# Kernel optimization log

Hardware: AMD Instinct MI355X
Metric: run time of the kernel (lower is better)

The kernel has to match this reference:

```python
import jax, jax.numpy as jnp
import numpy as np

B, S, D = 16, 512, 1024
H, HD = 16, 64          # head, head_dim; attn_dim = H*HD = D
FF = 4096               # linear_dim
EPS = 1e-6              # flax LayerNorm default epsilon


def _layernorm(x, scale):
    # flax LayerNorm(use_bias=False, use_scale=True)
    m = jnp.mean(x, axis=-1, keepdims=True)
    v = jnp.mean(jnp.square(x - m), axis=-1, keepdims=True)
    return (x - m) * jax.lax.rsqrt(v + EPS) * scale


def _attention(c, wq, wk, wv, wo):
    b, s, _ = c.shape
    q = (c @ wq).reshape(b, s, H, HD)
    k = (c @ wk).reshape(b, s, H, HD)
    v = (c @ wv).reshape(b, s, H, HD)
    score = jnp.einsum('bihd,bjhd->bijh', q, k) / jnp.sqrt(jnp.asarray(HD, c.dtype))
    score = jax.nn.softmax(score, axis=2)
    out = jnp.einsum('bijh,bjhd->bihd', score, v).reshape(b, s, H * HD)
    return out @ wo


def _mlp(x, w1, b1, w2, b2):
    return jax.nn.gelu(x @ w1 + b1) @ w2 + b2


def setup_inputs() -> dict:
    key = jax.random.key(0)
    ks = jax.random.split(key, 8)
    sd = 1.0 / np.sqrt(D)
    sf = 1.0 / np.sqrt(FF)
    return {
        'x': jax.random.normal(ks[0], (B, S, D), jnp.float32),
        'wq': jax.random.normal(ks[1], (D, D), jnp.float32) * sd,
        'wk': jax.random.normal(ks[2], (D, D), jnp.float32) * sd,
        'wv': jax.random.normal(ks[3], (D, D), jnp.float32) * sd,
        'wo': jax.random.normal(ks[4], (D, D), jnp.float32) * sd,
        'ln1_scale': jnp.ones((D,), jnp.float32),
        'ln2_scale': jnp.ones((D,), jnp.float32),
        'w1': jax.random.normal(ks[5], (D, FF), jnp.float32) * sd,
        'b1': jnp.zeros((FF,), jnp.float32),
        'w2': jax.random.normal(ks[6], (FF, D), jnp.float32) * sf,
        'b2': jnp.zeros((D,), jnp.float32),
    }


def reference(x, wq, wk, wv, wo, ln1_scale, ln2_scale, w1, b1, w2, b2):
    # inference mode: dropout / stochastic depth are identity
    c = _layernorm(x, ln1_scale)
    a = _attention(c, wq, wk, wv, wo)
    x = x + a           # x + dropout(attn(c,c))
    x = x + a           # x + attn(c,c)  (source adds attention output twice)
    x = x + _mlp(_layernorm(x, ln2_scale), w1, b1, w2, b2)
    x = x + _mlp(_layernorm(x, ln2_scale), w1, b1, w2, b2)
    return x
```

## Files before the change

### kernel.cpp

```cpp
#include <hip/hip_runtime.h>
#include <hip/hip_bf16.h>

typedef _Float16 f16;
typedef _Float16 f16x8 __attribute__((ext_vector_type(8)));
typedef _Float16 f16x4 __attribute__((ext_vector_type(4)));
typedef float    f32x4 __attribute__((ext_vector_type(4)));

#define MFMA16x16x32(a, b, c) __builtin_amdgcn_mfma_f32_16x16x32_f16(a, b, c, 0, 0, 0)

typedef __attribute__((address_space(1))) const void GASV;
typedef __attribute__((address_space(3))) void LASV;

#define WAIT_LGKM0 asm volatile("s_waitcnt lgkmcnt(0)" ::: "memory")
#define WAIT_VM2   asm volatile("s_waitcnt vmcnt(2)" ::: "memory")
#define WAIT_VM4   asm volatile("s_waitcnt vmcnt(4)" ::: "memory")

__device__ inline float gelu_f(float x) {
    float z = 0.79788456080286535588f * (x + 0.044715f * x * x * x);
    float e = __expf(2.0f * z);
    float t = 1.0f - 2.0f / (e + 1.0f);
    return 0.5f * x * (1.0f + t);
}

__global__ __launch_bounds__(256) void transpose_wt(const float* __restrict__ in,
                                                    f16* __restrict__ out,
                                                    int K, int N) {
    __shared__ float tile[32][33];
    int n0 = blockIdx.x * 32, k0 = blockIdx.y * 32;
    int tx = threadIdx.x & 31, ty = threadIdx.x >> 5;
#pragma unroll
    for (int i = 0; i < 32; i += 8)
        tile[ty + i][tx] = in[(size_t)(k0 + ty + i) * N + n0 + tx];
    __syncthreads();
#pragma unroll
    for (int i = 0; i < 32; i += 8)
        out[(size_t)(n0 + ty + i) * K + k0 + tx] = (f16)tile[tx][ty + i];
}

__global__ __launch_bounds__(256) void ln_f16(const float* __restrict__ x,
                                              const float* __restrict__ g,
                                              f16* __restrict__ out) {
    int row = blockIdx.x, t = threadIdx.x;
    float4 v = ((const float4*)(x + (size_t)row * 1024))[t];
    float s  = v.x + v.y + v.z + v.w;
    float s2 = v.x * v.x + v.y * v.y + v.z * v.z + v.w * v.w;
#pragma unroll
    for (int off = 1; off < 64; off <<= 1) {
        s  += __shfl_xor(s, off);
        s2 += __shfl_xor(s2, off);
    }
    __shared__ float red[8];
    int w = t >> 6, lane = t & 63;
    if (lane == 0) { red[w] = s; red[4 + w] = s2; }
    __syncthreads();
    s  = red[0] + red[1] + red[2] + red[3];
    s2 = red[4] + red[5] + red[6] + red[7];
    float mean = s * (1.0f / 1024.0f);
    float var  = s2 * (1.0f / 1024.0f) - mean * mean;
    float r = rsqrtf(var + 1e-6f);
    float4 gv = ((const float4*)g)[t];
    f16x4 ov;
    ov[0] = (f16)((v.x - mean) * r * gv.x);
    ov[1] = (f16)((v.y - mean) * r * gv.y);
    ov[2] = (f16)((v.z - mean) * r * gv.z);
    ov[3] = (f16)((v.w - mean) * r * gv.w);
    *(f16x4*)(out + (size_t)row * 1024 + t * 4) = ov;
}

template <int BM, int EPI>
__global__ __launch_bounds__(512, 2) void gemm8(
    const f16* __restrict__ A, const f16* __restrict__ Bt,
    const float* __restrict__ bias, const float* __restrict__ resid,
    float* __restrict__ outF, f16* __restrict__ outH,
    int M, int N, int K, float rscale) {
    static_assert(BM == 256 || BM == 128, "BM");
    constexpr int AH   = BM / 128;
    constexpr int MREP = BM / 32;
    constexpr int MH   = MREP / 2;

    __shared__ __align__(16) f16 lds[2][AH + 2][128 * 64];

    const int t512 = threadIdx.x;
    const int lane = t512 & 63, w = t512 >> 6;
    const int l15 = lane & 15, lg = lane >> 4;
    const int wr = w >> 2, wc = w & 3;

    const int nwg = gridDim.x;
    const int bid = blockIdx.x;
    const int swz = (bid & 7) * (nwg >> 3) + (bid >> 3);
    const int nbn = N >> 8;
    const int bm = swz / nbn, bn = swz % nbn;
    const int m0 = bm * BM, n0 = bn * 256;
    const int NT = K >> 6;

    const int ahalf = (BM == 256) ? wr : 0;
    const int arow0 = (BM == 256) ? 0 : wr * 64;
    const int bhalf = AH + (wc >> 1);
    const int brow0 = (wc & 1) * 64;

    auto stage = [&](int kt, int half) {
        if (kt >= NT) return;
        f16* dst0 = &lds[kt & 1][half][0];
        const bool isA = (half < AH);
        const f16* Mat = isA ? A : Bt;
        const int rb = isA ? (m0 + half * 128) : (n0 + (half - AH) * 128);
#pragma unroll
        for (int u = 0; u < 2; ++u) {
            int c = u * 512 + t512;
            int cs = c ^ ((c >> 3) & 7);
            const f16* src = Mat + (size_t)(rb + (cs >> 3)) * K + kt * 64 + (cs & 7) * 8;
            __builtin_amdgcn_global_load_lds((GASV*)src, (LASV*)(dst0 + c * 8), 16, 0, 0);
        }
    };
    auto ldfrag = [&](int cur, int half, int rh, int s) -> f16x8 {
        int ps = s ^ (rh & 7);
        return *(const f16x8*)(&lds[cur][half][0] + rh * 64 + ps * 8);
    };

    f32x4 acc[MREP][4] = {};
    f16x8 faL[2][MH], faH[2][MH], fb[2][4];

#pragma unroll
    for (int h = 0; h < AH + 2; ++h) stage(0, h);
#pragma unroll
    for (int h = 0; h < AH; ++h) stage(1, h);
    if (BM == 256) { WAIT_VM4; } else { WAIT_VM2; }
    __builtin_amdgcn_s_barrier();

    for (int t = 0; t < NT; ++t) {
        const int cur = t & 1;
#pragma unroll
        for (int ks = 0; ks < 2; ++ks) {
#pragma unroll
            for (int i = 0; i < MH; ++i) {
                int rh = arow0 + i * 16 + l15;
                faL[ks][i] = ldfrag(cur, ahalf, rh, ks * 4 + lg);
            }
#pragma unroll
            for (int j = 0; j < 2; ++j) {
                int rh = brow0 + j * 16 + l15;
                fb[ks][j] = ldfrag(cur, bhalf, rh, ks * 4 + lg);
            }
        }
        stage(t + 1, AH + 0);
        __builtin_amdgcn_s_barrier();
        WAIT_LGKM0;
        __builtin_amdgcn_s_setprio(1);
#pragma unroll
        for (int i = 0; i < MH; ++i)
#pragma unroll
            for (int j = 0; j < 2; ++j)
#pragma unroll
                for (int ks = 0; ks < 2; ++ks)
                    acc[i][j] = MFMA16x16x32(faL[ks][i], fb[ks][j], acc[i][j]);
        __builtin_amdgcn_s_setprio(0);
        __builtin_amdgcn_s_barrier();
#pragma unroll
        for (int ks = 0; ks < 2; ++ks)
#pragma unroll
            for (int j = 2; j < 4; ++j) {
                int rh = brow0 + j * 16 + l15;
                fb[ks][j] = ldfrag(cur, bhalf, rh, ks * 4 + lg);
            }
        stage(t + 1, AH + 1);
        __builtin_amdgcn_s_barrier();
        WAIT_LGKM0;
        __builtin_amdgcn_s_setprio(1);
#pragma unroll
        for (int i = 0; i < MH; ++i)
#pragma unroll
            for (int j = 0; j < 2; ++j)
#pragma unroll
                for (int ks = 0; ks < 2; ++ks)
                    acc[i][2 + j] = MFMA16x16x32(faL[ks][i], fb[ks][2 + j], acc[i][2 + j]);
        __builtin_amdgcn_s_setprio(0);
        __builtin_amdgcn_s_barrier();
#pragma unroll
        for (int ks = 0; ks < 2; ++ks)
#pragma unroll
            for (int i = 0; i < MH; ++i) {
                int rh = arow0 + (MH + i) * 16 + l15;
                faH[ks][i] = ldfrag(cur, ahalf, rh, ks * 4 + lg);
            }
        stage(t + 2, 0);
        __builtin_amdgcn_s_barrier();
        WAIT_LGKM0;
        __builtin_amdgcn_s_setprio(1);
#pragma unroll
        for (int i = 0; i < MH; ++i)
#pragma unroll
            for (int j = 0; j < 2; ++j)
#pragma unroll
                for (int ks = 0; ks < 2; ++ks)
                    acc[MH + i][j] = MFMA16x16x32(faH[ks][i], fb[ks][j], acc[MH + i][j]);
        __builtin_amdgcn_s_setprio(0);
        __builtin_amdgcn_s_barrier();
        if (AH == 2) stage(t + 2, 1);
        __builtin_amdgcn_s_barrier();
        WAIT_LGKM0;
        __builtin_amdgcn_s_setprio(1);
#pragma unroll
        for (int i = 0; i < MH; ++i)
#pragma unroll
            for (int j = 0; j < 2; ++j)
#pragma unroll
                for (int ks = 0; ks < 2; ++ks)
                    acc[MH + i][2 + j] = MFMA16x16x32(faH[ks][i], fb[ks][2 + j], acc[MH + i][2 + j]);
        __builtin_amdgcn_s_setprio(0);
        if (BM == 256) { WAIT_VM4; } else { WAIT_VM2; }
        __builtin_amdgcn_s_barrier();
    }

#pragma unroll
    for (int mi = 0; mi < MREP; ++mi) {
#pragma unroll
        for (int ni = 0; ni < 4; ++ni) {
            int colL = n0 + wc * 64 + ni * 16 + l15;
#pragma unroll
            for (int j = 0; j < 4; ++j) {
                int rowL = m0 + ((BM == 256) ? wr * 128 : wr * 64) + mi * 16 + lg * 4 + j;
                size_t idx = (size_t)rowL * N + colL;
                float vv = acc[mi][ni][j];
                if constexpr (EPI == 0) {
                    outH[idx] = (f16)vv;
                } else if constexpr (EPI == 1) {
                    vv += bias[colL];
                    outH[idx] = (f16)gelu_f(vv);
                } else if constexpr (EPI == 2) {
                    outF[idx] = resid[idx] + rscale * vv;
                } else {
                    outF[idx] = resid[idx] + vv + bias[colL];
                }
            }
        }
    }
}

__global__ __launch_bounds__(256) void attn_f16(const f16* __restrict__ qkv,
                                                int ld, f16* __restrict__ o) {
    __shared__ __align__(16) f16 Ks[512 * 64];
    __shared__ __align__(16) f16 Vt[64 * 512];
    __shared__ __align__(16) f16 Ps[4][16 * 32];

    const int t = threadIdx.x, lane = t & 63, w = t >> 6;
    const int l15 = lane & 15, lg = lane >> 4;
    const int bh = blockIdx.x, b = bh >> 4, h = bh & 15;
    const f16* qg = qkv + (size_t)(b * 512) * ld + h * 64;
    const f16* kg = qg + 1024;
    const f16* vg = qg + 2048;

#pragma unroll
    for (int i = 0; i < 16; ++i) {
        int c = i * 256 + t, r = c >> 3, s = c & 7;
        f16x8 val = *(const f16x8*)(kg + (size_t)r * ld + s * 8);
        *(f16x8*)((char*)Ks + r * 128 + ((s ^ (r & 7)) * 16)) = val;
    }
#pragma unroll
    for (int i = 0; i < 16; ++i) {
        int c = i * 256 + t, r = c >> 3, s = c & 7;
        f16x8 val = *(const f16x8*)(vg + (size_t)r * ld + s * 8);
#pragma unroll
        for (int dd = 0; dd < 8; ++dd) {
            int d = s * 8 + dd;
            *(f16*)((char*)Vt + d * 1024 + ((r * 2) ^ ((d & 7) << 4))) = val[dd];
        }
    }
    __syncthreads();

    for (int it = 0; it < 8; ++it) {
        int q0 = it * 64 + w * 16;
        f16x8 aq[2];
#pragma unroll
        for (int kk = 0; kk < 2; ++kk)
            aq[kk] = *(const f16x8*)(qg + (size_t)(q0 + l15) * ld + kk * 32 + lg * 8);

        f32x4 sc[32] = {};
#pragma unroll
        for (int jt = 0; jt < 32; ++jt) {
#pragma unroll
            for (int kk = 0; kk < 2; ++kk) {
                int row = jt * 16 + l15;
                f16x8 bk = *(const f16x8*)((char*)Ks + row * 128 + (((kk * 4 + lg) ^ (l15 & 7)) * 16));
                sc[jt] = MFMA16x16x32(aq[kk], bk, sc[jt]);
            }
        }

        float inv_sum[4];
#pragma unroll
        for (int r4 = 0; r4 < 4; ++r4) {
            float m = sc[0][r4];
#pragma unroll
            for (int jt = 1; jt < 32; ++jt) m = fmaxf(m, sc[jt][r4]);
#pragma unroll
            for (int off = 1; off < 16; off <<= 1) m = fmaxf(m, __shfl_xor(m, off));
            float sum = 0.0f;
#pragma unroll
            for (int jt = 0; jt < 32; ++jt) {
                float p = __expf((sc[jt][r4] - m) * 0.125f);
                sc[jt][r4] = p;
                sum += p;
            }
#pragma unroll
            for (int off = 1; off < 16; off <<= 1) sum += __shfl_xor(sum, off);
            inv_sum[r4] = 1.0f / sum;
        }

        f32x4 oa[4] = {};
        f16* myPs = &Ps[w][0];
#pragma unroll
        for (int u = 0; u < 16; ++u) {
#pragma unroll
            for (int half = 0; half < 2; ++half) {
                int jt = 2 * u + half;
#pragma unroll
                for (int r4 = 0; r4 < 4; ++r4) {
                    int row = lg * 4 + r4;
                    int colb = (half * 16 + l15) * 2;
                    *(f16*)((char*)myPs + row * 64 + (colb ^ (((row >> 1) & 3) << 4))) =
                        (f16)sc[jt][r4];
                }
            }
            f16x8 pa = *(const f16x8*)((char*)myPs + l15 * 64 + ((lg ^ ((l15 >> 1) & 3)) * 16));
#pragma unroll
            for (int ct = 0; ct < 4; ++ct) {
                int vrow = ct * 16 + l15;
                f16x8 bv = *(const f16x8*)((char*)Vt + vrow * 1024 + (((u * 4 + lg) ^ (vrow & 7)) * 16));
                oa[ct] = MFMA16x16x32(pa, bv, oa[ct]);
            }
        }

#pragma unroll
        for (int ct = 0; ct < 4; ++ct)
#pragma unroll
            for (int j = 0; j < 4; ++j) {
                int row = q0 + lg * 4 + j;
                int col = h * 64 + ct * 16 + l15;
                o[(size_t)(b * 512 + row) * 1024 + col] = (f16)(oa[ct][j] * inv_sum[j]);
            }
    }
}

extern "C" void kernel_launch(void* const* d_in, const int* in_sizes, int n_in,
                              void* d_out, int out_size, void* d_ws, size_t ws_size,
                              hipStream_t stream) {
    (void)in_sizes; (void)n_in; (void)out_size; (void)ws_size;
    const float* x   = (const float*)d_in[0];
    const float* wq  = (const float*)d_in[1];
    const float* wk  = (const float*)d_in[2];
    const float* wv  = (const float*)d_in[3];
    const float* wo  = (const float*)d_in[4];
    const float* ln1 = (const float*)d_in[5];
    const float* ln2 = (const float*)d_in[6];
    const float* w1  = (const float*)d_in[7];
    const float* b1  = (const float*)d_in[8];
    const float* w2  = (const float*)d_in[9];
    const float* b2  = (const float*)d_in[10];
    float* outF = (float*)d_out;

    char* ws = (char*)d_ws;
    size_t o = 0;
    f16* WqkvT = (f16*)(ws + o); o += (size_t)3072 * 1024 * 2;
    f16* WoT   = (f16*)(ws + o); o += (size_t)1024 * 1024 * 2;
    f16* W1T   = (f16*)(ws + o); o += (size_t)4096 * 1024 * 2;
    f16* W2T   = (f16*)(ws + o); o += (size_t)1024 * 4096 * 2;
    f16* cb    = (f16*)(ws + o); o += (size_t)8192 * 1024 * 2;
    f16* qkvb  = (f16*)(ws + o); o += (size_t)8192 * 3072 * 2;
    f16* hb    = (f16*)(ws + o); o += (size_t)8192 * 4096 * 2;
    float* x2  = (float*)(ws + o); o += (size_t)8192 * 1024 * 4;

    dim3 tb(256), tg(512);
    transpose_wt<<<dim3(32, 32), tb, 0, stream>>>(wq, WqkvT, 1024, 1024);
    transpose_wt<<<dim3(32, 32), tb, 0, stream>>>(wk, WqkvT + (size_t)1024 * 1024, 1024, 1024);
    transpose_wt<<<dim3(32, 32), tb, 0, stream>>>(wv, WqkvT + (size_t)2048 * 1024, 1024, 1024);
    transpose_wt<<<dim3(32, 32), tb, 0, stream>>>(wo, WoT, 1024, 1024);
    transpose_wt<<<dim3(128, 32), tb, 0, stream>>>(w1, W1T, 1024, 4096);
    transpose_wt<<<dim3(32, 128), tb, 0, stream>>>(w2, W2T, 4096, 1024);

    ln_f16<<<8192, tb, 0, stream>>>(x, ln1, cb);
    gemm8<256, 0><<<384, tg, 0, stream>>>(cb, WqkvT, nullptr, nullptr, nullptr, qkvb,
                                          8192, 3072, 1024, 0.f);
    attn_f16<<<256, tb, 0, stream>>>(qkvb, 3072, cb);
    gemm8<128, 2><<<256, tg, 0, stream>>>(cb, WoT, nullptr, x, outF, nullptr,
                                          8192, 1024, 1024, 2.0f);
    ln_f16<<<8192, tb, 0, stream>>>(outF, ln2, cb);
    gemm8<256, 1><<<512, tg, 0, stream>>>(cb, W1T, b1, nullptr, nullptr, hb,
                                          8192, 4096, 1024, 0.f);
    gemm8<128, 3><<<256, tg, 0, stream>>>(hb, W2T, b2, outF, x2, nullptr,
                                          8192, 1024, 4096, 1.0f);
    ln_f16<<<8192, tb, 0, stream>>>(x2, ln2, cb);
    gemm8<256, 1><<<512, tg, 0, stream>>>(cb, W1T, b1, nullptr, nullptr, hb,
                                          8192, 4096, 1024, 0.f);
    gemm8<128, 3><<<256, tg, 0, stream>>>(hb, W2T, b2, x2, outF, nullptr,
                                          8192, 1024, 4096, 1.0f);
}
```

Measured before the change: 665.0 us.

## Deepen GEMM prefetch to two K-tiles with uniform dummy loads and compile-time shapes

```diff
diff --git a/kernel.cpp b/kernel.cpp
--- a/kernel.cpp
+++ b/kernel.cpp
@@ -12,8 +12,8 @@
 typedef __attribute__((address_space(3))) void LASV;
 
 #define WAIT_LGKM0 asm volatile("s_waitcnt lgkmcnt(0)" ::: "memory")
-#define WAIT_VM2   asm volatile("s_waitcnt vmcnt(2)" ::: "memory")
-#define WAIT_VM4   asm volatile("s_waitcnt vmcnt(4)" ::: "memory")
+#define WAIT_VM6   asm volatile("s_waitcnt vmcnt(6)" ::: "memory")
+#define WAIT_VM8   asm volatile("s_waitcnt vmcnt(8)" ::: "memory")
 
 __device__ inline float gelu_f(float x) {
     float z = 0.79788456080286535588f * (x + 0.044715f * x * x * x);
@@ -67,18 +67,19 @@
     *(f16x4*)(out + (size_t)row * 1024 + t * 4) = ov;
 }
 
-template <int BM, int EPI>
+template <int BM, int EPI, int K, int N>
 __global__ __launch_bounds__(512, 2) void gemm8(
     const f16* __restrict__ A, const f16* __restrict__ Bt,
     const float* __restrict__ bias, const float* __restrict__ resid,
-    float* __restrict__ outF, f16* __restrict__ outH,
-    int M, int N, int K, float rscale) {
+    float* __restrict__ outF, f16* __restrict__ outH, float rscale) {
     static_assert(BM == 256 || BM == 128, "BM");
     constexpr int AH   = BM / 128;
     constexpr int MREP = BM / 32;
     constexpr int MH   = MREP / 2;
+    constexpr int NT   = K / 64;
 
     __shared__ __align__(16) f16 lds[2][AH + 2][128 * 64];
+    __shared__ __align__(16) f16 dummyb[8192];
 
     const int t512 = threadIdx.x;
     const int lane = t512 & 63, w = t512 >> 6;
@@ -88,10 +89,9 @@
     const int nwg = gridDim.x;
     const int bid = blockIdx.x;
     const int swz = (bid & 7) * (nwg >> 3) + (bid >> 3);
-    const int nbn = N >> 8;
+    constexpr int nbn = N / 256;
     const int bm = swz / nbn, bn = swz % nbn;
     const int m0 = bm * BM, n0 = bn * 256;
-    const int NT = K >> 6;
 
     const int ahalf = (BM == 256) ? wr : 0;
     const int arow0 = (BM == 256) ? 0 : wr * 64;
@@ -99,8 +99,8 @@
     const int brow0 = (wc & 1) * 64;
 
     auto stage = [&](int kt, int half) {
-        if (kt >= NT) return;
-        f16* dst0 = &lds[kt & 1][half][0];
+        const bool dum = (kt >= NT);
+        f16* dst0 = dum ? dummyb : &lds[kt & 1][half][0];
         const bool isA = (half < AH);
         const f16* Mat = isA ? A : Bt;
         const int rb = isA ? (m0 + half * 128) : (n0 + (half - AH) * 128);
@@ -108,7 +108,8 @@
         for (int u = 0; u < 2; ++u) {
             int c = u * 512 + t512;
             int cs = c ^ ((c >> 3) & 7);
-            const f16* src = Mat + (size_t)(rb + (cs >> 3)) * K + kt * 64 + (cs & 7) * 8;
+            const f16* src = dum ? (A + (size_t)(c & 511) * 8)
+                                 : (Mat + (size_t)(rb + (cs >> 3)) * K + kt * 64 + (cs & 7) * 8);
             __builtin_amdgcn_global_load_lds((GASV*)src, (LASV*)(dst0 + c * 8), 16, 0, 0);
         }
     };
@@ -123,8 +124,8 @@
 #pragma unroll
     for (int h = 0; h < AH + 2; ++h) stage(0, h);
 #pragma unroll
-    for (int h = 0; h < AH; ++h) stage(1, h);
-    if (BM == 256) { WAIT_VM4; } else { WAIT_VM2; }
+    for (int h = 0; h < AH + 2; ++h) stage(1, h);
+    if (BM == 256) { WAIT_VM8; } else { WAIT_VM6; }
     __builtin_amdgcn_s_barrier();
 
     for (int t = 0; t < NT; ++t) {
@@ -142,7 +143,6 @@
                 fb[ks][j] = ldfrag(cur, bhalf, rh, ks * 4 + lg);
             }
         }
-        stage(t + 1, AH + 0);
         __builtin_amdgcn_s_barrier();
         WAIT_LGKM0;
         __builtin_amdgcn_s_setprio(1);
@@ -162,7 +162,6 @@
                 int rh = brow0 + j * 16 + l15;
                 fb[ks][j] = ldfrag(cur, bhalf, rh, ks * 4 + lg);
             }
-        stage(t + 1, AH + 1);
         __builtin_amdgcn_s_barrier();
         WAIT_LGKM0;
         __builtin_amdgcn_s_setprio(1);
@@ -182,7 +181,7 @@
                 int rh = arow0 + (MH + i) * 16 + l15;
                 faH[ks][i] = ldfrag(cur, ahalf, rh, ks * 4 + lg);
             }
-        stage(t + 2, 0);
+        stage(t + 2, AH + 0);
         __builtin_amdgcn_s_barrier();
         WAIT_LGKM0;
         __builtin_amdgcn_s_setprio(1);
@@ -195,7 +194,9 @@
                     acc[MH + i][j] = MFMA16x16x32(faH[ks][i], fb[ks][j], acc[MH + i][j]);
         __builtin_amdgcn_s_setprio(0);
         __builtin_amdgcn_s_barrier();
-        if (AH == 2) stage(t + 2, 1);
+        stage(t + 2, AH + 1);
+#pragma unroll
+        for (int h = 0; h < AH; ++h) stage(t + 2, h);
         __builtin_amdgcn_s_barrier();
         WAIT_LGKM0;
         __builtin_amdgcn_s_setprio(1);
@@ -207,7 +208,7 @@
                 for (int ks = 0; ks < 2; ++ks)
                     acc[MH + i][2 + j] = MFMA16x16x32(faH[ks][i], fb[ks][2 + j], acc[MH + i][2 + j]);
         __builtin_amdgcn_s_setprio(0);
-        if (BM == 256) { WAIT_VM4; } else { WAIT_VM2; }
+        if (BM == 256) { WAIT_VM8; } else { WAIT_VM6; }
         __builtin_amdgcn_s_barrier();
     }
 
@@ -377,19 +378,19 @@
     transpose_wt<<<dim3(32, 128), tb, 0, stream>>>(w2, W2T, 4096, 1024);
 
     ln_f16<<<8192, tb, 0, stream>>>(x, ln1, cb);
-    gemm8<256, 0><<<384, tg, 0, stream>>>(cb, WqkvT, nullptr, nullptr, nullptr, qkvb,
-                                          8192, 3072, 1024, 0.f);
+    gemm8<256, 0, 1024, 3072><<<384, tg, 0, stream>>>(cb, WqkvT, nullptr, nullptr,
+                                                      nullptr, qkvb, 0.f);
     attn_f16<<<256, tb, 0, stream>>>(qkvb, 3072, cb);
-    gemm8<128, 2><<<256, tg, 0, stream>>>(cb, WoT, nullptr, x, outF, nullptr,
-                                          8192, 1024, 1024, 2.0f);
+    gemm8<128, 2, 1024, 1024><<<256, tg, 0, stream>>>(cb, WoT, nullptr, x,
+                                                      outF, nullptr, 2.0f);
     ln_f16<<<8192, tb, 0, stream>>>(outF, ln2, cb);
-    gemm8<256, 1><<<512, tg, 0, stream>>>(cb, W1T, b1, nullptr, nullptr, hb,
-                                          8192, 4096, 1024, 0.f);
-    gemm8<128, 3><<<256, tg, 0, stream>>>(hb, W2T, b2, outF, x2, nullptr,
-                                          8192, 1024, 4096, 1.0f);
+    gemm8<256, 1, 1024, 4096><<<512, tg, 0, stream>>>(cb, W1T, b1, nullptr,
+                                                      nullptr, hb, 0.f);
+    gemm8<128, 3, 4096, 1024><<<256, tg, 0, stream>>>(hb, W2T, b2, outF,
+                                                      x2, nullptr, 1.0f);
     ln_f16<<<8192, tb, 0, stream>>>(x2, ln2, cb);
-    gemm8<256, 1><<<512, tg, 0, stream>>>(cb, W1T, b1, nullptr, nullptr, hb,
-                                          8192, 4096, 1024, 0.f);
-    gemm8<128, 3><<<256, tg, 0, stream>>>(hb, W2T, b2, x2, outF, nullptr,
-                                          8192, 1024, 4096, 1.0f);
-}
+    gemm8<256, 1, 1024, 4096><<<512, tg, 0, stream>>>(cb, W1T, b1, nullptr,
+                                                      nullptr, hb, 0.f);
+    gemm8<128, 3, 4096, 1024><<<256, tg, 0, stream>>>(hb, W2T, b2, x2,
+                                                      outF, nullptr, 1.0f);
+}
```

Result: slower. 678.5 us (+2.0%).
